# Optimization experiments

Hardware: AMD Instinct MI355X
Metric: run time of the kernel (lower is better)

## Reference

```python
import jax, jax.numpy as jnp
import numpy as np

N, E = 50000, 1_000_000
IN_F, OUT_F = 128, 64
NEG_SLOPE = 0.2


def setup_inputs() -> dict:
    key = jax.random.key(0)
    k1, k2, k3, k4, k5 = jax.random.split(key, 5)
    x = jax.random.normal(k1, (N, IN_F), dtype=jnp.float32)
    edge_index = jax.random.randint(k2, (2, E), 0, N, dtype=jnp.int64)
    # xavier_uniform with gain=1.414 (as in the torch init)
    gain = 1.414
    bW = gain * np.sqrt(6.0 / (IN_F + OUT_F))
    W = jax.random.uniform(k3, (IN_F, OUT_F), jnp.float32, -bW, bW)
    ba = gain * np.sqrt(6.0 / (OUT_F + 1))
    a_src = jax.random.uniform(k4, (OUT_F, 1), jnp.float32, -ba, ba)
    a_dst = jax.random.uniform(k5, (OUT_F, 1), jnp.float32, -ba, ba)
    return {"x": x, "edge_index": edge_index, "W": W, "a_src": a_src, "a_dst": a_dst}


def reference(x, edge_index, W, a_src, a_dst):
    n = x.shape[0]
    Wh = x @ W                                  # [N, F_out]
    src = edge_index[0]
    dst = edge_index[1]
    # per-edge attention logits: (Wh[src] . a_src) + (Wh[dst] . a_dst)
    s_src = Wh @ a_src[:, 0]                    # [N]
    s_dst = Wh @ a_dst[:, 0]                    # [N]
    e = jax.nn.leaky_relu(s_src[src] + s_dst[dst], negative_slope=NEG_SLOPE)  # [E]
    e = jnp.exp(e - jnp.max(e))                 # global-max stabilized exp (matches torch code)
    denom = jax.ops.segment_sum(e, dst, num_segments=n) + 1e-16  # [N]
    alpha = e / denom[dst]                      # [E]  (dropout p=0 -> identity)
    out = jax.ops.segment_sum(Wh[src] * alpha[:, None], dst, num_segments=n)  # [N, F_out]
    return jax.nn.elu(out)
```

## Files before the change

kernel.cpp:

```cpp
#include <hip/hip_runtime.h>
#include <hip/hip_bf16.h>
#include <math.h>

#define NN 50000
#define NE 1000000
#define FIN 128
#define FOUT 64
#define NEG 0.2f

#define NB   2048
#define DPB  25
#define NBUSED 2000
#define TS   4096
#define NT   245
#define NTP  256
#define RCAP 1024
#define TILE_BLKS 245
#define GEMM_BLKS 391

using short8  = __attribute__((ext_vector_type(8))) short;
using floatx4 = __attribute__((ext_vector_type(4))) float;

static __device__ __forceinline__ short f2bf(float f) {
    __hip_bfloat16 h = __float2bfloat16(f);
    return *(short*)&h;
}

__global__ __launch_bounds__(512) void k_front(
    const float* __restrict__ x, const float* __restrict__ W,
    const float* __restrict__ a_src, const float* __restrict__ a_dst,
    const int* __restrict__ ei,
    __hip_bfloat16* __restrict__ Whb, float* __restrict__ s_src,
    float* __restrict__ s_dst,
    unsigned* __restrict__ bdata, int* __restrict__ gofs)
{
    __shared__ int cnt[NB];
    __shared__ int cur[NB];
    __shared__ unsigned srt[TS];
    __shared__ int wsum[8];

    const int tid  = threadIdx.x;
    const int lane = tid & 63;
    const int wv   = tid >> 6;

    if (blockIdx.x >= TILE_BLKS) {
        const int col  = lane & 15;
        const int quad = lane >> 4;
        const int strip = (blockIdx.x - TILE_BLKS) * 8 + wv;
        if (strip >= NN / 16) return;
        const int row0 = strip * 16;

        short8 bfr[4][4];
        #pragma unroll
        for (int kk = 0; kk < 4; ++kk) {
            #pragma unroll
            for (int nt = 0; nt < 4; ++nt) {
                const float* wp = W + (kk * 32 + quad * 8) * FOUT + nt * 16 + col;
                #pragma unroll
                for (int j = 0; j < 8; ++j)
                    bfr[kk][nt][j] = f2bf(wp[j * FOUT]);
            }
        }

        floatx4 acc[4] = {{0.f,0.f,0.f,0.f},{0.f,0.f,0.f,0.f},
                          {0.f,0.f,0.f,0.f},{0.f,0.f,0.f,0.f}};

        const float* xrow = x + (size_t)(row0 + col) * FIN + quad * 8;
        #pragma unroll
        for (int kk = 0; kk < 4; ++kk) {
            const float4 u0 = *(const float4*)(xrow + kk * 32);
            const float4 u1 = *(const float4*)(xrow + kk * 32 + 4);
            short8 af;
            af[0] = f2bf(u0.x); af[1] = f2bf(u0.y);
            af[2] = f2bf(u0.z); af[3] = f2bf(u0.w);
            af[4] = f2bf(u1.x); af[5] = f2bf(u1.y);
            af[6] = f2bf(u1.z); af[7] = f2bf(u1.w);
            #pragma unroll
            for (int nt = 0; nt < 4; ++nt)
                acc[nt] = __builtin_amdgcn_mfma_f32_16x16x32_bf16(
                    af, bfr[kk][nt], acc[nt], 0, 0, 0);
        }

        const float av0 = a_src[col], av1 = a_src[16 + col];
        const float av2 = a_src[32 + col], av3 = a_src[48 + col];
        const float bv0 = a_dst[col], bv1 = a_dst[16 + col];
        const float bv2 = a_dst[32 + col], bv3 = a_dst[48 + col];

        float ps[4], pd[4];
        #pragma unroll
        for (int reg = 0; reg < 4; ++reg) {
            ps[reg] = acc[0][reg] * av0 + acc[1][reg] * av1
                    + acc[2][reg] * av2 + acc[3][reg] * av3;
            pd[reg] = acc[0][reg] * bv0 + acc[1][reg] * bv1
                    + acc[2][reg] * bv2 + acc[3][reg] * bv3;
        }

        #pragma unroll
        for (int nt = 0; nt < 4; ++nt)
            #pragma unroll
            for (int reg = 0; reg < 4; ++reg)
                Whb[(size_t)(row0 + quad * 4 + reg) * FOUT + nt * 16 + col] =
                    __float2bfloat16(acc[nt][reg]);

        #pragma unroll
        for (int off = 1; off < 16; off <<= 1) {
            #pragma unroll
            for (int reg = 0; reg < 4; ++reg) {
                ps[reg] += __shfl_xor(ps[reg], off);
                pd[reg] += __shfl_xor(pd[reg], off);
            }
        }
        if (col == 0) {
            #pragma unroll
            for (int reg = 0; reg < 4; ++reg) {
                s_src[row0 + quad * 4 + reg] = ps[reg];
                s_dst[row0 + quad * 4 + reg] = pd[reg];
            }
        }
        return;
    }

    const int tile = blockIdx.x;
    const int base = tile * TS;
    const int tcnt = (NE - base < TS) ? (NE - base) : TS;

    for (int i = tid; i < NB; i += 512) cnt[i] = 0;
    __syncthreads();

    unsigned pk[8];
    #pragma unroll
    for (int j = 0; j < 8; ++j) {
        const int i = j * 512 + tid;
        if (i < tcnt) {
            const int e = base + i;
            const unsigned s = (unsigned)__builtin_nontemporal_load(ei + e);
            const unsigned d = (unsigned)__builtin_nontemporal_load(ei + NE + e);
            pk[j] = (s << 16) | d;
            atomicAdd(&cnt[d / DPB], 1);
        } else pk[j] = 0xFFFFFFFFu;
    }
    __syncthreads();

    {
        const int i0 = tid * 4;
        const int v0 = cnt[i0], v1 = cnt[i0 + 1];
        const int v2 = cnt[i0 + 2], v3 = cnt[i0 + 3];
        const int s = v0 + v1 + v2 + v3;
        int inc = s;
        #pragma unroll
        for (int off = 1; off < 64; off <<= 1) {
            const int t = __shfl_up(inc, off);
            if (lane >= off) inc += t;
        }
        if (lane == 63) wsum[wv] = inc;
        __syncthreads();
        int wb = 0;
        #pragma unroll
        for (int w = 0; w < 7; ++w) if (w < wv) wb += wsum[w];
        const int excl = wb + inc - s;
        cur[i0]     = excl;
        cur[i0 + 1] = excl + v0;
        cur[i0 + 2] = excl + v0 + v1;
        cur[i0 + 3] = excl + v0 + v1 + v2;
        *(int4*)(gofs + (size_t)tile * NB + i0) =
            make_int4(excl, excl + v0, excl + v0 + v1, excl + v0 + v1 + v2);
    }
    __syncthreads();

    #pragma unroll
    for (int j = 0; j < 8; ++j) {
        if (pk[j] != 0xFFFFFFFFu) {
            const int b = (int)(pk[j] & 0xffffu) / DPB;
            const int pos = atomicAdd(&cur[b], 1);
            srt[pos] = pk[j];
        }
    }
    __syncthreads();

    for (int i = tid; i < tcnt; i += 512)
        bdata[base + i] = srt[i];
}

__global__ __launch_bounds__(256) void k_transp(
    const int* __restrict__ gofs, int* __restrict__ gofs_t)
{
    __shared__ int tb[32][33];
    const int bi = blockIdx.x & 63;
    const int ti = blockIdx.x >> 6;
    const int r = threadIdx.x >> 5;
    const int c = threadIdx.x & 31;
    for (int rr = r; rr < 32; rr += 8) {
        const int t = ti * 32 + rr;
        tb[rr][c] = (t < NT) ? gofs[(size_t)t * NB + bi * 32 + c] : 0;
    }
    __syncthreads();
    for (int rr = r; rr < 32; rr += 8) {
        const int b = bi * 32 + rr;
        gofs_t[(size_t)b * NTP + ti * 32 + c] = tb[c][rr];
    }
}

__global__ __launch_bounds__(256) void k_sortgather(
    const int* __restrict__ gofs_t, const unsigned* __restrict__ bdata,
    const float* __restrict__ s_src, const float* __restrict__ s_dst,
    const __hip_bfloat16* __restrict__ Whb, float* __restrict__ out)
{
    __shared__ unsigned raw[RCAP];
    __shared__ uint2 pes[RCAP];
    __shared__ float sdl[32];
    __shared__ int cnt[32];
    __shared__ int ofs2[33];
    __shared__ int cur[32];
    __shared__ int wsum[4];

    const int b = (blockIdx.x & 7) * 250 + (blockIdx.x >> 3);
    const int tid = threadIdx.x;
    const int lane = tid & 63;
    const int wv = tid >> 6;
    const int d0 = b * DPB;

    if (tid < 32) {
        cnt[tid] = 0;
        sdl[tid] = (tid < DPB) ? s_dst[d0 + tid] : 0.f;
    }

    int c = 0, o = 0;
    if (tid < NT) {
        o = gofs_t[(size_t)b * NTP + tid];
        c = gofs_t[(size_t)(b + 1) * NTP + tid] - o;
    }
    int inc = c;
    #pragma unroll
    for (int off = 1; off < 64; off <<= 1) {
        const int t = __shfl_up(inc, off);
        if (lane >= off) inc += t;
    }
    if (lane == 63) wsum[wv] = inc;
    __syncthreads();
    int wb = 0;
    #pragma unroll
    for (int w = 0; w < 3; ++w) if (w < wv) wb += wsum[w];
    const int segbase = wb + inc - c;
    int tot = wsum[0] + wsum[1] + wsum[2] + wsum[3];
    if (tot > RCAP) tot = RCAP;

    for (int k = 0; k < c; ++k) {
        const int p = segbase + k;
        if (p < RCAP) raw[p] = bdata[(size_t)tid * TS + o + k];
    }
    __syncthreads();

    for (int i = tid; i < tot; i += 256)
        atomicAdd(&cnt[(int)(raw[i] & 0xffffu) - d0], 1);
    __syncthreads();

    if (tid < 32) {
        const int cc = (tid < DPB) ? cnt[tid] : 0;
        int in2 = cc;
        #pragma unroll
        for (int off = 1; off < 32; off <<= 1) {
            const int t = __shfl_up(in2, off);
            if (tid >= off) in2 += t;
        }
        ofs2[tid + 1] = in2;
        if (tid == 0) ofs2[0] = 0;
        cur[tid] = in2 - cc;
    }
    __syncthreads();

    for (int i = tid; i < tot; i += 256) {
        const unsigned p = raw[i];
        const int j = (int)(p & 0xffffu) - d0;
        const int pos = atomicAdd(&cur[j], 1);
        float v = s_src[p >> 16] + sdl[j];
        v = (v > 0.f) ? v : NEG * v;
        pes[pos] = make_uint2(p, __float_as_uint(__expf(v)));
    }
    __syncthreads();

    const int h  = lane >> 5;
    const int l5 = lane & 31;
    for (int j = wv; j < DPB; j += 4) {
        const int d = d0 + j;
        const int beg = ofs2[j];
        const int end = ofs2[j + 1];
        float a0 = 0.f, a1 = 0.f, dacc = 0.f;
        int i = beg;
        for (; i + 8 <= end; i += 8) {
            #pragma unroll
            for (int k = 0; k < 4; ++k) {
                const uint2 q = pes[i + 2 * k + h];
                const float ev = __uint_as_float(q.y);
                const unsigned u = ((const unsigned*)(Whb +
                        (size_t)(q.x >> 16) * FOUT))[l5];
                const float f0 = __uint_as_float(u << 16);
                const float f1 = __uint_as_float(u & 0xffff0000u);
                a0 = fmaf(ev, f0, a0);
                a1 = fmaf(ev, f1, a1);
                dacc += ev;
            }
        }
        for (; i + 2 <= end; i += 2) {
            const uint2 q = pes[i + h];
            const float ev = __uint_as_float(q.y);
            const unsigned u = ((const unsigned*)(Whb +
                    (size_t)(q.x >> 16) * FOUT))[l5];
            a0 = fmaf(ev, __uint_as_float(u << 16), a0);
            a1 = fmaf(ev, __uint_as_float(u & 0xffff0000u), a1);
            dacc += ev;
        }
        if (i < end && h == 0) {
            const uint2 q = pes[i];
            const float ev = __uint_as_float(q.y);
            const unsigned u = ((const unsigned*)(Whb +
                    (size_t)(q.x >> 16) * FOUT))[l5];
            a0 = fmaf(ev, __uint_as_float(u << 16), a0);
            a1 = fmaf(ev, __uint_as_float(u & 0xffff0000u), a1);
            dacc += ev;
        }
        a0 += __shfl_xor(a0, 32);
        a1 += __shfl_xor(a1, 32);
        dacc += __shfl_xor(dacc, 32);
        if (h == 0) {
            const float rd = 1.f / (dacc + 1e-16f);
            float r0 = a0 * rd, r1 = a1 * rd;
            r0 = (r0 > 0.f) ? r0 : expm1f(r0);
            r1 = (r1 > 0.f) ? r1 : expm1f(r1);
            ((float2*)(out + (size_t)d * FOUT))[l5] = make_float2(r0, r1);
        }
    }
}

extern "C" void kernel_launch(void* const* d_in, const int* in_sizes, int n_in,
                              void* d_out, int out_size, void* d_ws, size_t ws_size,
                              hipStream_t stream)
{
    const float* x     = (const float*)d_in[0];
    const int*   ei    = (const int*)d_in[1];
    const float* W     = (const float*)d_in[2];
    const float* a_src = (const float*)d_in[3];
    const float* a_dst = (const float*)d_in[4];
    float* out = (float*)d_out;

    float* ws    = (float*)d_ws;
    __hip_bfloat16* Whb = (__hip_bfloat16*)ws;
    float* s_src = ws + (size_t)NN * FOUT / 2;
    float* s_dst = s_src + NN;
    int*   gofs  = (int*)(s_dst + NN);
    int*   gofs_t = gofs + (size_t)NT * NB;
    unsigned* bdata = (unsigned*)(gofs_t + (size_t)NB * NTP);

    k_front<<<TILE_BLKS + GEMM_BLKS, 512, 0, stream>>>(
        x, W, a_src, a_dst, ei, Whb, s_src, s_dst, bdata, gofs);
    k_transp<<<512, 256, 0, stream>>>(gofs, gofs_t);
    k_sortgather<<<NBUSED, 256, 0, stream>>>(gofs_t, bdata, s_src, s_dst,
                                             Whb, out);
}
```

Before: 122.2 us.

## Write transposed offsets directly and drop the transpose kernel, plus load tweaks

The front kernel now writes per-tile bucket offsets straight into the transposed layout, which removes the separate transpose kernel launch and its global round trip. The scattered strided stores are less coalesced. The change also adds non-temporal loads of x and non-temporal stores of the output. The edge record now holds a precomputed byte offset, which simplifies the gather address math, and the raw-copy loop bound is clamped outside the loop.

```diff
diff --git a/kernel.cpp b/kernel.cpp
--- a/kernel.cpp
+++ b/kernel.cpp
@@ -20,6 +20,7 @@
 
 using short8  = __attribute__((ext_vector_type(8))) short;
 using floatx4 = __attribute__((ext_vector_type(4))) float;
+using floatx2 = __attribute__((ext_vector_type(2))) float;
 
 static __device__ __forceinline__ short f2bf(float f) {
     __hip_bfloat16 h = __float2bfloat16(f);
@@ -32,7 +33,7 @@
     const int* __restrict__ ei,
     __hip_bfloat16* __restrict__ Whb, float* __restrict__ s_src,
     float* __restrict__ s_dst,
-    unsigned* __restrict__ bdata, int* __restrict__ gofs)
+    unsigned* __restrict__ bdata, int* __restrict__ gofs_t)
 {
     __shared__ int cnt[NB];
     __shared__ int cur[NB];
@@ -68,13 +69,15 @@
         const float* xrow = x + (size_t)(row0 + col) * FIN + quad * 8;
         #pragma unroll
         for (int kk = 0; kk < 4; ++kk) {
-            const float4 u0 = *(const float4*)(xrow + kk * 32);
-            const float4 u1 = *(const float4*)(xrow + kk * 32 + 4);
+            const floatx4 u0 = __builtin_nontemporal_load(
+                (const floatx4*)(xrow + kk * 32));
+            const floatx4 u1 = __builtin_nontemporal_load(
+                (const floatx4*)(xrow + kk * 32 + 4));
             short8 af;
-            af[0] = f2bf(u0.x); af[1] = f2bf(u0.y);
-            af[2] = f2bf(u0.z); af[3] = f2bf(u0.w);
-            af[4] = f2bf(u1.x); af[5] = f2bf(u1.y);
-            af[6] = f2bf(u1.z); af[7] = f2bf(u1.w);
+            af[0] = f2bf(u0[0]); af[1] = f2bf(u0[1]);
+            af[2] = f2bf(u0[2]); af[3] = f2bf(u0[3]);
+            af[4] = f2bf(u1[0]); af[5] = f2bf(u1[1]);
+            af[6] = f2bf(u1[2]); af[7] = f2bf(u1[3]);
             #pragma unroll
             for (int nt = 0; nt < 4; ++nt)
                 acc[nt] = __builtin_amdgcn_mfma_f32_16x16x32_bf16(
@@ -162,8 +165,11 @@
         cur[i0 + 1] = excl + v0;
         cur[i0 + 2] = excl + v0 + v1;
         cur[i0 + 3] = excl + v0 + v1 + v2;
-        *(int4*)(gofs + (size_t)tile * NB + i0) =
-            make_int4(excl, excl + v0, excl + v0 + v1, excl + v0 + v1 + v2);
+        int* gt = gofs_t + tile;
+        gt[(size_t)i0 * NTP]       = excl;
+        gt[(size_t)(i0 + 1) * NTP] = excl + v0;
+        gt[(size_t)(i0 + 2) * NTP] = excl + v0 + v1;
+        gt[(size_t)(i0 + 3) * NTP] = excl + v0 + v1 + v2;
     }
     __syncthreads();
 
@@ -179,25 +185,6 @@
 
     for (int i = tid; i < tcnt; i += 512)
         bdata[base + i] = srt[i];
-}
-
-__global__ __launch_bounds__(256) void k_transp(
-    const int* __restrict__ gofs, int* __restrict__ gofs_t)
-{
-    __shared__ int tb[32][33];
-    const int bi = blockIdx.x & 63;
-    const int ti = blockIdx.x >> 6;
-    const int r = threadIdx.x >> 5;
-    const int c = threadIdx.x & 31;
-    for (int rr = r; rr < 32; rr += 8) {
-        const int t = ti * 32 + rr;
-        tb[rr][c] = (t < NT) ? gofs[(size_t)t * NB + bi * 32 + c] : 0;
-    }
-    __syncthreads();
-    for (int rr = r; rr < 32; rr += 8) {
-        const int b = bi * 32 + rr;
-        gofs_t[(size_t)b * NTP + ti * 32 + c] = tb[c][rr];
-    }
 }
 
 __global__ __launch_bounds__(256) void k_sortgather(
@@ -244,9 +231,11 @@
     int tot = wsum[0] + wsum[1] + wsum[2] + wsum[3];
     if (tot > RCAP) tot = RCAP;
 
-    for (int k = 0; k < c; ++k) {
-        const int p = segbase + k;
-        if (p < RCAP) raw[p] = bdata[(size_t)tid * TS + o + k];
+    {
+        const unsigned* bsrc = bdata + (size_t)tid * TS + o;
+        int lim = RCAP - segbase; if (lim > c) lim = c; if (lim < 0) lim = 0;
+        for (int k = 0; k < lim; ++k)
+            raw[segbase + k] = bsrc[k];
     }
     __syncthreads();
 
@@ -274,12 +263,14 @@
         const int pos = atomicAdd(&cur[j], 1);
         float v = s_src[p >> 16] + sdl[j];
         v = (v > 0.f) ? v : NEG * v;
-        pes[pos] = make_uint2(p, __float_as_uint(__expf(v)));
+        pes[pos] = make_uint2((p & 0xffff0000u) >> 9,
+                              __float_as_uint(__expf(v)));
     }
     __syncthreads();
 
     const int h  = lane >> 5;
     const int l5 = lane & 31;
+    const char* wbase = (const char*)Whb + (l5 << 2);
     for (int j = wv; j < DPB; j += 4) {
         const int d = d0 + j;
         const int beg = ofs2[j];
@@ -291,8 +282,7 @@
             for (int k = 0; k < 4; ++k) {
                 const uint2 q = pes[i + 2 * k + h];
                 const float ev = __uint_as_float(q.y);
-                const unsigned u = ((const unsigned*)(Whb +
-                        (size_t)(q.x >> 16) * FOUT))[l5];
+                const unsigned u = *(const unsigned*)(wbase + q.x);
                 const float f0 = __uint_as_float(u << 16);
                 const float f1 = __uint_as_float(u & 0xffff0000u);
                 a0 = fmaf(ev, f0, a0);
@@ -303,8 +293,7 @@
         for (; i + 2 <= end; i += 2) {
             const uint2 q = pes[i + h];
             const float ev = __uint_as_float(q.y);
-            const unsigned u = ((const unsigned*)(Whb +
-                    (size_t)(q.x >> 16) * FOUT))[l5];
+            const unsigned u = *(const unsigned*)(wbase + q.x);
             a0 = fmaf(ev, __uint_as_float(u << 16), a0);
             a1 = fmaf(ev, __uint_as_float(u & 0xffff0000u), a1);
             dacc += ev;
@@ -312,8 +301,7 @@
         if (i < end && h == 0) {
             const uint2 q = pes[i];
             const float ev = __uint_as_float(q.y);
-            const unsigned u = ((const unsigned*)(Whb +
-                    (size_t)(q.x >> 16) * FOUT))[l5];
+            const unsigned u = *(const unsigned*)(wbase + q.x);
             a0 = fmaf(ev, __uint_as_float(u << 16), a0);
             a1 = fmaf(ev, __uint_as_float(u & 0xffff0000u), a1);
             dacc += ev;
@@ -326,7 +314,9 @@
             float r0 = a0 * rd, r1 = a1 * rd;
             r0 = (r0 > 0.f) ? r0 : expm1f(r0);
             r1 = (r1 > 0.f) ? r1 : expm1f(r1);
-            ((float2*)(out + (size_t)d * FOUT))[l5] = make_float2(r0, r1);
+            floatx2 rr; rr[0] = r0; rr[1] = r1;
+            __builtin_nontemporal_store(
+                rr, (floatx2*)(out + (size_t)d * FOUT) + l5);
         }
     }
 }
@@ -346,13 +336,11 @@
     __hip_bfloat16* Whb = (__hip_bfloat16*)ws;
     float* s_src = ws + (size_t)NN * FOUT / 2;
     float* s_dst = s_src + NN;
-    int*   gofs  = (int*)(s_dst + NN);
-    int*   gofs_t = gofs + (size_t)NT * NB;
+    int*   gofs_t = (int*)(s_dst + NN);
     unsigned* bdata = (unsigned*)(gofs_t + (size_t)NB * NTP);
 
     k_front<<<TILE_BLKS + GEMM_BLKS, 512, 0, stream>>>(
-        x, W, a_src, a_dst, ei, Whb, s_src, s_dst, bdata, gofs);
-    k_transp<<<512, 256, 0, stream>>>(gofs, gofs_t);
+        x, W, a_src, a_dst, ei, Whb, s_src, s_dst, bdata, gofs_t);
     k_sortgather<<<NBUSED, 256, 0, stream>>>(gofs_t, bdata, s_src, s_dst,
                                              Whb, out);
 }
```

Result: slower. 125.1 us (+2.3%).
